# Kernel optimization log

Measured on AMD Instinct MI355X. Metric: run time of the kernel, lower is better.

## Reference

```python
import jax, jax.numpy as jnp
import numpy as np

C = 256
HEADS = 8
HEAD_DIM = C // HEADS
GROUPS = 8
EPS = 1e-5


def setup_inputs() -> dict:
    key = jax.random.key(0)
    ks = jax.random.split(key, 11)
    B, S = 2, 16
    s = 0.02
    return {
        "x": jax.random.normal(ks[0], (B, C, S, S, S), dtype=jnp.float32),
        "gn_w": jnp.ones((C,), jnp.float32),
        "gn_b": jnp.zeros((C,), jnp.float32),
        "wq": jax.random.normal(ks[1], (C, C), jnp.float32) * s,
        "bq": jnp.zeros((C,), jnp.float32),
        "wk": jax.random.normal(ks[2], (C, C), jnp.float32) * s,
        "bk": jnp.zeros((C,), jnp.float32),
        "wv": jax.random.normal(ks[3], (C, C), jnp.float32) * s,
        "bv": jnp.zeros((C,), jnp.float32),
        "wo": jax.random.normal(ks[4], (C, C), jnp.float32) * s,
        "bo": jnp.zeros((C,), jnp.float32),
    }


def _group_norm(x, w, b):
    # x: [B, C, D, H, W]; GroupNorm(8, C) with affine params
    B, Cc, D, H, W = x.shape
    xg = x.reshape(B, GROUPS, Cc // GROUPS, D, H, W)
    mu = jnp.mean(xg, axis=(2, 3, 4, 5), keepdims=True)
    var = jnp.mean(jnp.square(xg - mu), axis=(2, 3, 4, 5), keepdims=True)
    xn = ((xg - mu) * jax.lax.rsqrt(var + EPS)).reshape(B, Cc, D, H, W)
    return xn * w[None, :, None, None, None] + b[None, :, None, None, None]


def reference(x, gn_w, gn_b, wq, bq, wk, bk, wv, bv, wo, bo):
    B, Cc, D, H, W = x.shape
    N = D * H * W
    xn = _group_norm(x, gn_w, gn_b).reshape(B, Cc, N)  # [B,C,N]
    # 1x1x1 Conv3d == per-voxel linear: weight [out,in]
    Q = jnp.einsum("oc,bcn->bon", wq, xn) + bq[None, :, None]
    K = jnp.einsum("oc,bcn->bon", wk, xn) + bk[None, :, None]
    V = jnp.einsum("oc,bcn->bon", wv, xn) + bv[None, :, None]
    Q = Q.reshape(B, HEADS, HEAD_DIM, N)
    K = K.reshape(B, HEADS, HEAD_DIM, N)
    V = V.reshape(B, HEADS, HEAD_DIM, N)
    scale = np.sqrt(HEAD_DIM).astype(np.float32)
    attn = jnp.einsum("bhdn,bhdm->bhnm", Q, K) / scale
    attn = jax.nn.softmax(attn, axis=-1)
    out = jnp.einsum("bhnm,bhdm->bhdn", attn, V)  # [B,h,hd,N]
    out = out.reshape(B, Cc, N)
    out = jnp.einsum("oc,bcn->bon", wo, out) + bo[None, :, None]
    return x + out.reshape(B, Cc, D, H, W)
```

## Files before the change

### kernel.cpp

```cpp
#include <hip/hip_runtime.h>

#define B_   2
#define C_   256
#define N_   4096
#define H_   8
#define HD_  32
#define G_   8
#define CPG_ 32

typedef short short8 __attribute__((ext_vector_type(8)));
typedef short short4v __attribute__((ext_vector_type(4)));
typedef unsigned uint4v __attribute__((ext_vector_type(4)));
typedef float f32x4  __attribute__((ext_vector_type(4)));
typedef float f4     __attribute__((ext_vector_type(4)));

__device__ __forceinline__ float b2f(short s) {
    return __uint_as_float(((unsigned)(unsigned short)s) << 16);
}
__device__ __forceinline__ short f2b(float f) {
    unsigned u = __float_as_uint(f);
    unsigned r = (u + 0x7FFF + ((u >> 16) & 1)) >> 16;
    return (short)r;
}

__global__ __launch_bounds__(256) void gn_part(const float* __restrict__ x,
                                               float* __restrict__ part) {
    int blk = blockIdx.x;
    const f4* p = (const f4*)x + (size_t)(blk >> 6) * (CPG_ * N_ / 4) + (size_t)(blk & 63) * 512;
    float s = 0.f, ss = 0.f;
#pragma unroll
    for (int i = 0; i < 2; i++) {
        f4 v = p[threadIdx.x + i * 256];
#pragma unroll
        for (int j = 0; j < 4; j++) { float f = v[j]; s += f; ss += f * f; }
    }
#pragma unroll
    for (int off = 32; off > 0; off >>= 1) {
        s  += __shfl_down(s, off);
        ss += __shfl_down(ss, off);
    }
    __shared__ float rs[4], rss[4];
    int w = threadIdx.x >> 6;
    if ((threadIdx.x & 63) == 0) { rs[w] = s; rss[w] = ss; }
    __syncthreads();
    if (threadIdx.x == 0) {
        part[blk * 2]     = rs[0] + rs[1] + rs[2] + rs[3];
        part[blk * 2 + 1] = rss[0] + rss[1] + rss[2] + rss[3];
    }
}

__global__ __launch_bounds__(256) void wconv(const float* __restrict__ wq,
                                             const float* __restrict__ wk,
                                             const float* __restrict__ wv,
                                             const float* __restrict__ wo,
                                             short* __restrict__ wb) {
    int gid = blockIdx.x * 256 + threadIdx.x;
    int rid = gid >> 13;
    int off = (gid & 8191) * 8;
    const float* src = rid == 0 ? wq : (rid == 1 ? wk : (rid == 2 ? wv : wo));
    f4 a = *(const f4*)(src + off);
    f4 b = *(const f4*)(src + off + 4);
    short8 r;
#pragma unroll
    for (int j = 0; j < 4; j++) { r[j] = f2b(a[j]); r[j + 4] = f2b(b[j]); }
    *(short8*)&wb[(size_t)rid * 65536 + off] = r;
}

__global__ __launch_bounds__(256, 2) void gemm_qkv(
    const float* __restrict__ x,
    const float* __restrict__ gw, const float* __restrict__ gb,
    const float* __restrict__ part,
    const short* __restrict__ wb,
    const float* __restrict__ bq, const float* __restrict__ bk,
    const float* __restrict__ bv,
    short* __restrict__ q, short* __restrict__ kt, short* __restrict__ v) {
    int b = blockIdx.z;
    int o0 = blockIdx.y * 64, n0 = blockIdx.x * 64;
    const float mul = 0.17677669529663687f * 1.4426950408889634f;

    __shared__ short wl[3][64][40];
    __shared__ short xl[64][40];
    __shared__ float ga[256], gbb[256];
    __shared__ float mus[8], rstds[8];

    int tid = threadIdx.x;
    int w = tid >> 6, lane = tid & 63, li = lane & 15, quad = lane >> 4;
    int wr = w & 1, wc = w >> 1;

#pragma unroll
    for (int gi = 0; gi < 2; gi++) {
        int g = w * 2 + gi;
        const float* pp = &part[(size_t)(b * 8 + g) * 128 + lane * 2];
        float s = pp[0], ss = pp[1];
#pragma unroll
        for (int off = 32; off > 0; off >>= 1) {
            s  += __shfl_down(s, off);
            ss += __shfl_down(ss, off);
        }
        if (lane == 0) {
            const float inv = 1.f / (float)(CPG_ * N_);
            float mu = s * inv;
            float var = ss * inv - mu * mu;
            mus[g] = mu;
            rstds[g] = rsqrtf(var + 1e-5f);
        }
    }
    __syncthreads();
    {
        int c = tid, g = c >> 5;
        float a = rstds[g] * gw[c];
        ga[c]  = a;
        gbb[c] = gb[c] - mus[g] * a;
    }

    f32x4 aq[2][2], ak[2][2], av[2][2];
#pragma unroll
    for (int i = 0; i < 2; i++)
#pragma unroll
        for (int j = 0; j < 2; j++) {
            aq[i][j] = (f32x4){0.f, 0.f, 0.f, 0.f};
            ak[i][j] = (f32x4){0.f, 0.f, 0.f, 0.f};
            av[i][j] = (f32x4){0.f, 0.f, 0.f, 0.f};
        }

    int wrow = tid >> 2, wco = (tid & 3) << 3;
    int cpair = tid >> 4, l16 = tid & 15;
    __syncthreads();

    for (int k0 = 0; k0 < 256; k0 += 32) {
#pragma unroll
        for (int m = 0; m < 3; m++)
            *(short8*)&wl[m][wrow][wco] =
                *(const short8*)&wb[(size_t)m * 65536 + (size_t)(o0 + wrow) * 256 + k0 + wco];
        {
            int c0 = k0 + cpair * 2;
            float a0 = ga[c0],     b0c = gbb[c0];
            float a1 = ga[c0 + 1], b1c = gbb[c0 + 1];
            const float* xr0 = x + ((size_t)(b * 256 + c0)) * N_ + n0 + l16;
            const float* xr1 = xr0 + N_;
#pragma unroll
            for (int j = 0; j < 4; j++) {
                unsigned lo = (unsigned short)f2b(xr0[16 * j] * a0 + b0c);
                unsigned hi = (unsigned short)f2b(xr1[16 * j] * a1 + b1c);
                *(unsigned*)&xl[l16 + 16 * j][cpair * 2] = lo | (hi << 16);
            }
        }
        __syncthreads();

        short8 xf[2];
#pragma unroll
        for (int i = 0; i < 2; i++)
            xf[i] = *(short8*)&xl[wc * 32 + i * 16 + li][quad * 8];
#pragma unroll
        for (int j = 0; j < 2; j++) {
            short8 wfq = *(short8*)&wl[0][wr * 32 + j * 16 + li][quad * 8];
            short8 wfk = *(short8*)&wl[1][wr * 32 + j * 16 + li][quad * 8];
            short8 wfv = *(short8*)&wl[2][wr * 32 + j * 16 + li][quad * 8];
#pragma unroll
            for (int i = 0; i < 2; i++) {
                aq[i][j] = __builtin_amdgcn_mfma_f32_16x16x32_bf16(xf[i], wfq, aq[i][j], 0, 0, 0);
                ak[i][j] = __builtin_amdgcn_mfma_f32_16x16x32_bf16(xf[i], wfk, ak[i][j], 0, 0, 0);
                av[j][i] = __builtin_amdgcn_mfma_f32_16x16x32_bf16(wfv, xf[i], av[j][i], 0, 0, 0);
            }
        }
        __syncthreads();
    }

    {
        short* outp = q + (size_t)b * N_ * C_;
#pragma unroll
        for (int i = 0; i < 2; i++) {
            int nb_ = n0 + wc * 32 + i * 16 + quad * 4;
#pragma unroll
            for (int j = 0; j < 2; j++) {
                int o_ = o0 + wr * 32 + j * 16 + li;
                float bv_ = bq[o_];
#pragma unroll
                for (int r = 0; r < 4; r++)
                    outp[(size_t)(nb_ + r) * C_ + o_] = f2b((aq[i][j][r] + bv_) * mul);
            }
        }
    }
    {
#pragma unroll
        for (int i = 0; i < 2; i++) {
            int nb_ = n0 + wc * 32 + i * 16 + quad * 4;
#pragma unroll
            for (int j = 0; j < 2; j++) {
                int o_ = o0 + wr * 32 + j * 16 + li;
                int hh = o_ >> 5, d = o_ & 31;
                float bv_ = bk[o_];
                short* kdst = kt + ((size_t)(b * 8 + hh) * N_) * HD_ + d;
#pragma unroll
                for (int r = 0; r < 4; r++)
                    kdst[(size_t)(nb_ + r) * HD_] = f2b(ak[i][j][r] + bv_);
            }
        }
    }
    {
        short* outp = v + (size_t)b * C_ * N_;
#pragma unroll
        for (int j = 0; j < 2; j++) {
            int ob = o0 + wr * 32 + j * 16 + quad * 4;
#pragma unroll
            for (int i = 0; i < 2; i++) {
                int n_ = n0 + wc * 32 + i * 16 + li;
#pragma unroll
                for (int r = 0; r < 4; r++)
                    outp[(size_t)(ob + r) * N_ + n_] = f2b(av[j][i][r] + bv[ob + r]);
            }
        }
    }
}

__global__ __launch_bounds__(512) void flash(const short* __restrict__ q,
                                             const short* __restrict__ ktp,
                                             const short* __restrict__ v,
                                             short* __restrict__ aoT) {
    int bid = blockIdx.x;
    int xcd = bid & 7;
    int rest = bid >> 3;
    int bh = xcd * 2 + (rest & 1);
    int nb = rest >> 1;
    int b = bh >> 3, h = bh & 7;

    const short* QT = q   + (size_t)b * N_ * C_ + h * HD_;
    const short* KP = ktp + (size_t)bh * N_ * HD_;
    const short* V  = v   + ((size_t)b * C_ + h * HD_) * N_;
    short* O = aoT + (size_t)b * N_ * C_ + h * HD_;

    __shared__ short kl[2 * 2560];
    __shared__ short vl[2 * 2304];

    int tid = threadIdx.x, w = tid >> 6, lane = tid & 63, li = lane & 15, quad = lane >> 4;
    int n0w = nb * 256 + w * 32;

    short8 qf0 = *(const short8*)&QT[(size_t)(n0w + li) * 256 + quad * 8];
    short8 qf1 = *(const short8*)&QT[(size_t)(n0w + 16 + li) * 256 + quad * 8];

    f32x4 oa00 = (f32x4){0.f,0.f,0.f,0.f}, oa01 = oa00, oa10 = oa00, oa11 = oa00;
    float lr0 = 0.f, lr1 = 0.f;
    const f32x4 zero = (f32x4){0.f, 0.f, 0.f, 0.f};

    int krow = tid >> 3, kcol = (tid & 7) << 2;
    const short* kgp = KP + (size_t)krow * HD_ + kcol;
    int klo = krow * 40 + kcol;
    int vd = tid >> 4, g = tid & 15;
    int mbase = 32 * (g >> 3) + 16 * (g & 1) + 4 * ((g >> 1) & 3);
    const short* vgp = V + (size_t)vd * N_ + mbase;
    int vlo = vd * 72 + g * 4;

    short4v kst = *(const short4v*)kgp;
    short4v vst = *(const short4v*)vgp;

    f32x4 s0[4], s1[4];
    short8 vf[4];

    for (int t = 0; t < 64; ++t) {
        int buf = t & 1;
        *(short4v*)&kl[buf * 2560 + klo] = kst;
        *(short4v*)&vl[buf * 2304 + vlo] = vst;
        if (t < 63) {
            kst = *(const short4v*)(kgp + (size_t)(t + 1) * 64 * HD_);
            vst = *(const short4v*)(vgp + (t + 1) * 64);
        }
        __syncthreads();

        __builtin_amdgcn_s_setprio(1);
#pragma unroll
        for (int c = 0; c < 4; c++) {
            short8 kf = *(short8*)&kl[buf * 2560 + (c * 16 + li) * 40 + quad * 8];
            s0[c] = __builtin_amdgcn_mfma_f32_16x16x32_bf16(kf, qf0, zero, 0, 0, 0);
            s1[c] = __builtin_amdgcn_mfma_f32_16x16x32_bf16(kf, qf1, zero, 0, 0, 0);
        }
        __builtin_amdgcn_s_setprio(0);

        vf[0] = *(short8*)&vl[buf * 2304 + li * 72 + quad * 8];
        vf[1] = *(short8*)&vl[buf * 2304 + (16 + li) * 72 + quad * 8];
        vf[2] = *(short8*)&vl[buf * 2304 + li * 72 + 32 + quad * 8];
        vf[3] = *(short8*)&vl[buf * 2304 + (16 + li) * 72 + 32 + quad * 8];

        unsigned paw[8];
        float lp = 0.f;
#pragma unroll
        for (int c = 0; c < 4; c++) {
            float e0 = __builtin_amdgcn_exp2f(s0[c][0]);
            float e1 = __builtin_amdgcn_exp2f(s0[c][1]);
            float e2 = __builtin_amdgcn_exp2f(s0[c][2]);
            float e3 = __builtin_amdgcn_exp2f(s0[c][3]);
            lp += (e0 + e1) + (e2 + e3);
            paw[2 * c]     = __builtin_amdgcn_perm(__float_as_uint(e1), __float_as_uint(e0), 0x07060302);
            paw[2 * c + 1] = __builtin_amdgcn_perm(__float_as_uint(e3), __float_as_uint(e2), 0x07060302);
        }
        lr0 += lp;
        uint4v p0 = (uint4v){paw[0], paw[1], paw[2], paw[3]};
        uint4v p1 = (uint4v){paw[4], paw[5], paw[6], paw[7]};
        short8 a0 = __builtin_bit_cast(short8, p0);
        short8 a1 = __builtin_bit_cast(short8, p1);

        lp = 0.f;
#pragma unroll
        for (int c = 0; c < 4; c++) {
            float e0 = __builtin_amdgcn_exp2f(s1[c][0]);
            float e1 = __builtin_amdgcn_exp2f(s1[c][1]);
            float e2 = __builtin_amdgcn_exp2f(s1[c][2]);
            float e3 = __builtin_amdgcn_exp2f(s1[c][3]);
            lp += (e0 + e1) + (e2 + e3);
            paw[2 * c]     = __builtin_amdgcn_perm(__float_as_uint(e1), __float_as_uint(e0), 0x07060302);
            paw[2 * c + 1] = __builtin_amdgcn_perm(__float_as_uint(e3), __float_as_uint(e2), 0x07060302);
        }
        lr1 += lp;
        uint4v p2 = (uint4v){paw[0], paw[1], paw[2], paw[3]};
        uint4v p3 = (uint4v){paw[4], paw[5], paw[6], paw[7]};
        short8 a2 = __builtin_bit_cast(short8, p2);
        short8 a3 = __builtin_bit_cast(short8, p3);

        __builtin_amdgcn_s_setprio(1);
        oa00 = __builtin_amdgcn_mfma_f32_16x16x32_bf16(a0, vf[0], oa00, 0, 0, 0);
        oa01 = __builtin_amdgcn_mfma_f32_16x16x32_bf16(a0, vf[1], oa01, 0, 0, 0);
        oa00 = __builtin_amdgcn_mfma_f32_16x16x32_bf16(a1, vf[2], oa00, 0, 0, 0);
        oa01 = __builtin_amdgcn_mfma_f32_16x16x32_bf16(a1, vf[3], oa01, 0, 0, 0);
        oa10 = __builtin_amdgcn_mfma_f32_16x16x32_bf16(a2, vf[0], oa10, 0, 0, 0);
        oa11 = __builtin_amdgcn_mfma_f32_16x16x32_bf16(a2, vf[1], oa11, 0, 0, 0);
        oa10 = __builtin_amdgcn_mfma_f32_16x16x32_bf16(a3, vf[2], oa10, 0, 0, 0);
        oa11 = __builtin_amdgcn_mfma_f32_16x16x32_bf16(a3, vf[3], oa11, 0, 0, 0);
        __builtin_amdgcn_s_setprio(0);
    }

    lr0 += __shfl_xor(lr0, 16); lr0 += __shfl_xor(lr0, 32);
    lr1 += __shfl_xor(lr1, 16); lr1 += __shfl_xor(lr1, 32);
#pragma unroll
    for (int r = 0; r < 4; r++) {
        float ln0 = __shfl(lr0, quad * 4 + r);
        float inv0 = 1.f / ln0;
        size_t n_ = (size_t)(n0w + quad * 4 + r);
        O[n_ * 256 + li]      = f2b(oa00[r] * inv0);
        O[n_ * 256 + 16 + li] = f2b(oa01[r] * inv0);
        float ln1 = __shfl(lr1, quad * 4 + r);
        float inv1 = 1.f / ln1;
        size_t n2 = (size_t)(n0w + 16 + quad * 4 + r);
        O[n2 * 256 + li]      = f2b(oa10[r] * inv1);
        O[n2 * 256 + 16 + li] = f2b(oa11[r] * inv1);
    }
}

__global__ __launch_bounds__(256) void gemm_out(const short* __restrict__ wob,
                                                const float* __restrict__ bias,
                                                const short* __restrict__ aoT,
                                                const float* __restrict__ resid,
                                                float* __restrict__ out) {
    int b = blockIdx.z;
    const short* X = aoT + (size_t)b * N_ * C_;
    const float* R = resid + (size_t)b * C_ * N_;
    float* outp = out + (size_t)b * C_ * N_;

    __shared__ short wl[64][40];
    __shared__ short xl[64][40];

    int o0 = blockIdx.y * 64, n0 = blockIdx.x * 64;
    int tid = threadIdx.x;
    int w = tid >> 6, lane = tid & 63, li = lane & 15, quad = lane >> 4;
    int wr = w & 1, wc = w >> 1;

    f32x4 acc[2][2];
#pragma unroll
    for (int i = 0; i < 2; i++)
#pragma unroll
        for (int j = 0; j < 2; j++) acc[i][j] = (f32x4){0.f, 0.f, 0.f, 0.f};

    int row = tid >> 2, co = (tid & 3) << 3;
    for (int k0 = 0; k0 < 256; k0 += 32) {
        *(short8*)&wl[row][co] = *(const short8*)&wob[(size_t)(o0 + row) * 256 + k0 + co];
        *(short8*)&xl[row][co] = *(const short8*)&X[(size_t)(n0 + row) * 256 + k0 + co];
        __syncthreads();
        short8 af[2], bfr[2];
#pragma unroll
        for (int i = 0; i < 2; i++) af[i]  = *(short8*)&wl[wr * 32 + i * 16 + li][quad * 8];
#pragma unroll
        for (int j = 0; j < 2; j++) bfr[j] = *(short8*)&xl[wc * 32 + j * 16 + li][quad * 8];
#pragma unroll
        for (int i = 0; i < 2; i++)
#pragma unroll
            for (int j = 0; j < 2; j++)
                acc[i][j] = __builtin_amdgcn_mfma_f32_16x16x32_bf16(af[i], bfr[j], acc[i][j], 0, 0, 0);
        __syncthreads();
    }
#pragma unroll
    for (int i = 0; i < 2; i++) {
        int ob = o0 + wr * 32 + i * 16 + quad * 4;
#pragma unroll
        for (int j = 0; j < 2; j++) {
            int n_ = n0 + wc * 32 + j * 16 + li;
#pragma unroll
            for (int r = 0; r < 4; r++) {
                size_t idx = (size_t)(ob + r) * N_ + n_;
                outp[idx] = acc[i][j][r] + bias[ob + r] + R[idx];
            }
        }
    }
}

extern "C" void kernel_launch(void* const* d_in, const int* in_sizes, int n_in,
                              void* d_out, int out_size, void* d_ws, size_t ws_size,
                              hipStream_t stream) {
    const float* x  = (const float*)d_in[0];
    const float* gw = (const float*)d_in[1];
    const float* gb = (const float*)d_in[2];
    const float* wq = (const float*)d_in[3];
    const float* bq = (const float*)d_in[4];
    const float* wk = (const float*)d_in[5];
    const float* bk = (const float*)d_in[6];
    const float* wv = (const float*)d_in[7];
    const float* bv = (const float*)d_in[8];
    const float* wo = (const float*)d_in[9];
    const float* bo = (const float*)d_in[10];
    float* out = (float*)d_out;

    char* ws = (char*)d_ws;
    float* part = (float*)ws;
    const size_t TS = (size_t)B_ * N_ * C_;
    short* aoT = (short*)(ws + 16384);
    short* q   = aoT + TS;
    short* kt  = q + TS;
    short* v   = kt + TS;
    short* wb  = v + TS;

    gn_part<<<1024, 256, 0, stream>>>(x, part);
    wconv<<<128, 256, 0, stream>>>(wq, wk, wv, wo, wb);
    gemm_qkv<<<dim3(64, 4, 2), 256, 0, stream>>>(x, gw, gb, part, wb,
                                                 bq, bk, bv, q, kt, v);
    flash<<<256, 512, 0, stream>>>(q, kt, v, aoT);
    gemm_out<<<dim3(64, 4, 2), 256, 0, stream>>>(wb + 3 * 65536, bo, aoT, x, out);
}
```

Baseline: 147.7 us.

## Merge GN stats and weight conversion kernels; process two key tiles per flash iteration

Merges the group-norm partial-sum kernel and the weight bf16 conversion into one launch, branching on block index. In the flash attention kernel, each loop iteration now stages two 64-key tiles (128 keys) with double buffering, halving the number of barriers and iterations. The QK MFMAs for both tiles are issued back to back, and the second tile's exp/PV work can then overlap with them. It also adds a launch bound requesting 2 blocks per CU. The cost is doubled LDS use per block and higher register pressure from the extra score accumulators.

Result: no change. 147.2 us (-0.3%).

```diff
diff --git a/kernel.cpp b/kernel.cpp
--- a/kernel.cpp
+++ b/kernel.cpp
@@ -23,47 +23,48 @@
     return (short)r;
 }
 
-__global__ __launch_bounds__(256) void gn_part(const float* __restrict__ x,
-                                               float* __restrict__ part) {
+__global__ __launch_bounds__(256) void prep(const float* __restrict__ x,
+                                            float* __restrict__ part,
+                                            const float* __restrict__ wq,
+                                            const float* __restrict__ wk,
+                                            const float* __restrict__ wv,
+                                            const float* __restrict__ wo,
+                                            short* __restrict__ wb) {
     int blk = blockIdx.x;
-    const f4* p = (const f4*)x + (size_t)(blk >> 6) * (CPG_ * N_ / 4) + (size_t)(blk & 63) * 512;
-    float s = 0.f, ss = 0.f;
-#pragma unroll
-    for (int i = 0; i < 2; i++) {
-        f4 v = p[threadIdx.x + i * 256];
-#pragma unroll
-        for (int j = 0; j < 4; j++) { float f = v[j]; s += f; ss += f * f; }
-    }
-#pragma unroll
-    for (int off = 32; off > 0; off >>= 1) {
-        s  += __shfl_down(s, off);
-        ss += __shfl_down(ss, off);
-    }
-    __shared__ float rs[4], rss[4];
-    int w = threadIdx.x >> 6;
-    if ((threadIdx.x & 63) == 0) { rs[w] = s; rss[w] = ss; }
-    __syncthreads();
-    if (threadIdx.x == 0) {
-        part[blk * 2]     = rs[0] + rs[1] + rs[2] + rs[3];
-        part[blk * 2 + 1] = rss[0] + rss[1] + rss[2] + rss[3];
-    }
-}
-
-__global__ __launch_bounds__(256) void wconv(const float* __restrict__ wq,
-                                             const float* __restrict__ wk,
-                                             const float* __restrict__ wv,
-                                             const float* __restrict__ wo,
-                                             short* __restrict__ wb) {
-    int gid = blockIdx.x * 256 + threadIdx.x;
-    int rid = gid >> 13;
-    int off = (gid & 8191) * 8;
-    const float* src = rid == 0 ? wq : (rid == 1 ? wk : (rid == 2 ? wv : wo));
-    f4 a = *(const f4*)(src + off);
-    f4 b = *(const f4*)(src + off + 4);
-    short8 r;
-#pragma unroll
-    for (int j = 0; j < 4; j++) { r[j] = f2b(a[j]); r[j + 4] = f2b(b[j]); }
-    *(short8*)&wb[(size_t)rid * 65536 + off] = r;
+    if (blk < 1024) {
+        const f4* p = (const f4*)x + (size_t)(blk >> 6) * (CPG_ * N_ / 4) + (size_t)(blk & 63) * 512;
+        float s = 0.f, ss = 0.f;
+#pragma unroll
+        for (int i = 0; i < 2; i++) {
+            f4 v = p[threadIdx.x + i * 256];
+#pragma unroll
+            for (int j = 0; j < 4; j++) { float f = v[j]; s += f; ss += f * f; }
+        }
+#pragma unroll
+        for (int off = 32; off > 0; off >>= 1) {
+            s  += __shfl_down(s, off);
+            ss += __shfl_down(ss, off);
+        }
+        __shared__ float rs[4], rss[4];
+        int w = threadIdx.x >> 6;
+        if ((threadIdx.x & 63) == 0) { rs[w] = s; rss[w] = ss; }
+        __syncthreads();
+        if (threadIdx.x == 0) {
+            part[blk * 2]     = rs[0] + rs[1] + rs[2] + rs[3];
+            part[blk * 2 + 1] = rss[0] + rss[1] + rss[2] + rss[3];
+        }
+    } else {
+        int gid = (blk - 1024) * 256 + threadIdx.x;
+        int rid = gid >> 13;
+        int off = (gid & 8191) * 8;
+        const float* src = rid == 0 ? wq : (rid == 1 ? wk : (rid == 2 ? wv : wo));
+        f4 a = *(const f4*)(src + off);
+        f4 b = *(const f4*)(src + off + 4);
+        short8 r;
+#pragma unroll
+        for (int j = 0; j < 4; j++) { r[j] = f2b(a[j]); r[j + 4] = f2b(b[j]); }
+        *(short8*)&wb[(size_t)rid * 65536 + off] = r;
+    }
 }
 
 __global__ __launch_bounds__(256, 2) void gemm_qkv(
@@ -213,10 +214,31 @@
     }
 }
 
-__global__ __launch_bounds__(512) void flash(const short* __restrict__ q,
-                                             const short* __restrict__ ktp,
-                                             const short* __restrict__ v,
-                                             short* __restrict__ aoT) {
+#define EXPPACK(sx, lrx, A0, A1)                                          \
+    {                                                                     \
+        unsigned paw[8];                                                  \
+        float lp = 0.f;                                                   \
+        _Pragma("unroll")                                                 \
+        for (int c = 0; c < 4; c++) {                                     \
+            float e0 = __builtin_amdgcn_exp2f(sx[c][0]);                  \
+            float e1 = __builtin_amdgcn_exp2f(sx[c][1]);                  \
+            float e2 = __builtin_amdgcn_exp2f(sx[c][2]);                  \
+            float e3 = __builtin_amdgcn_exp2f(sx[c][3]);                  \
+            lp += (e0 + e1) + (e2 + e3);                                  \
+            paw[2 * c]     = __builtin_amdgcn_perm(__float_as_uint(e1), __float_as_uint(e0), 0x07060302); \
+            paw[2 * c + 1] = __builtin_amdgcn_perm(__float_as_uint(e3), __float_as_uint(e2), 0x07060302); \
+        }                                                                 \
+        lrx += lp;                                                        \
+        uint4v p0_ = (uint4v){paw[0], paw[1], paw[2], paw[3]};            \
+        uint4v p1_ = (uint4v){paw[4], paw[5], paw[6], paw[7]};            \
+        A0 = __builtin_bit_cast(short8, p0_);                             \
+        A1 = __builtin_bit_cast(short8, p1_);                             \
+    }
+
+__global__ __launch_bounds__(512, 2) void flash(const short* __restrict__ q,
+                                                const short* __restrict__ ktp,
+                                                const short* __restrict__ v,
+                                                short* __restrict__ aoT) {
     int bid = blockIdx.x;
     int xcd = bid & 7;
     int rest = bid >> 3;
@@ -229,8 +251,8 @@
     const short* V  = v   + ((size_t)b * C_ + h * HD_) * N_;
     short* O = aoT + (size_t)b * N_ * C_ + h * HD_;
 
-    __shared__ short kl[2 * 2560];
-    __shared__ short vl[2 * 2304];
+    __shared__ short kl[2 * 5120];
+    __shared__ short vl[2 * 4608];
 
     int tid = threadIdx.x, w = tid >> 6, lane = tid & 63, li = lane & 15, quad = lane >> 4;
     int n0w = nb * 256 + w * 32;
@@ -250,70 +272,72 @@
     const short* vgp = V + (size_t)vd * N_ + mbase;
     int vlo = vd * 72 + g * 4;
 
-    short4v kst = *(const short4v*)kgp;
-    short4v vst = *(const short4v*)vgp;
-
-    f32x4 s0[4], s1[4];
+    short4v kstA = *(const short4v*)kgp;
+    short4v kstB = *(const short4v*)(kgp + (size_t)64 * HD_);
+    short4v vstA = *(const short4v*)vgp;
+    short4v vstB = *(const short4v*)(vgp + 64);
+
+    f32x4 s0a[4], s1a[4], s0b[4], s1b[4];
     short8 vf[4];
 
-    for (int t = 0; t < 64; ++t) {
+    for (int t = 0; t < 32; ++t) {
         int buf = t & 1;
-        *(short4v*)&kl[buf * 2560 + klo] = kst;
-        *(short4v*)&vl[buf * 2304 + vlo] = vst;
-        if (t < 63) {
-            kst = *(const short4v*)(kgp + (size_t)(t + 1) * 64 * HD_);
-            vst = *(const short4v*)(vgp + (t + 1) * 64);
+        *(short4v*)&kl[buf * 5120 + klo] = kstA;
+        *(short4v*)&kl[buf * 5120 + 2560 + klo] = kstB;
+        *(short4v*)&vl[buf * 4608 + vlo] = vstA;
+        *(short4v*)&vl[buf * 4608 + 2304 + vlo] = vstB;
+        if (t < 31) {
+            const short* kq = kgp + (size_t)(t + 1) * 128 * HD_;
+            kstA = *(const short4v*)kq;
+            kstB = *(const short4v*)(kq + (size_t)64 * HD_);
+            const short* vq = vgp + (t + 1) * 128;
+            vstA = *(const short4v*)vq;
+            vstB = *(const short4v*)(vq + 64);
         }
         __syncthreads();
 
         __builtin_amdgcn_s_setprio(1);
 #pragma unroll
         for (int c = 0; c < 4; c++) {
-            short8 kf = *(short8*)&kl[buf * 2560 + (c * 16 + li) * 40 + quad * 8];
-            s0[c] = __builtin_amdgcn_mfma_f32_16x16x32_bf16(kf, qf0, zero, 0, 0, 0);
-            s1[c] = __builtin_amdgcn_mfma_f32_16x16x32_bf16(kf, qf1, zero, 0, 0, 0);
+            short8 kf = *(short8*)&kl[buf * 5120 + (c * 16 + li) * 40 + quad * 8];
+            s0a[c] = __builtin_amdgcn_mfma_f32_16x16x32_bf16(kf, qf0, zero, 0, 0, 0);
+            s1a[c] = __builtin_amdgcn_mfma_f32_16x16x32_bf16(kf, qf1, zero, 0, 0, 0);
+        }
+#pragma unroll
+        for (int c = 0; c < 4; c++) {
+            short8 kf = *(short8*)&kl[buf * 5120 + 2560 + (c * 16 + li) * 40 + quad * 8];
+            s0b[c] = __builtin_amdgcn_mfma_f32_16x16x32_bf16(kf, qf0, zero, 0, 0, 0);
+            s1b[c] = __builtin_amdgcn_mfma_f32_16x16x32_bf16(kf, qf1, zero, 0, 0, 0);
         }
         __builtin_amdgcn_s_setprio(0);
 
-        vf[0] = *(short8*)&vl[buf * 2304 + li * 72 + quad * 8];
-        vf[1] = *(short8*)&vl[buf * 2304 + (16 + li) * 72 + quad * 8];
-        vf[2] = *(short8*)&vl[buf * 2304 + li * 72 + 32 + quad * 8];
-        vf[3] = *(short8*)&vl[buf * 2304 + (16 + li) * 72 + 32 + quad * 8];
-
-        unsigned paw[8];
-        float lp = 0.f;
-#pragma unroll
-        for (int c = 0; c < 4; c++) {
-            float e0 = __builtin_amdgcn_exp2f(s0[c][0]);
-            float e1 = __builtin_amdgcn_exp2f(s0[c][1]);
-            float e2 = __builtin_amdgcn_exp2f(s0[c][2]);
-            float e3 = __builtin_amdgcn_exp2f(s0[c][3]);
-            lp += (e0 + e1) + (e2 + e3);
-            paw[2 * c]     = __builtin_amdgcn_perm(__float_as_uint(e1), __float_as_uint(e0), 0x07060302);
-            paw[2 * c + 1] = __builtin_amdgcn_perm(__float_as_uint(e3), __float_as_uint(e2), 0x07060302);
-        }
-        lr0 += lp;
-        uint4v p0 = (uint4v){paw[0], paw[1], paw[2], paw[3]};
-        uint4v p1 = (uint4v){paw[4], paw[5], paw[6], paw[7]};
-        short8 a0 = __builtin_bit_cast(short8, p0);
-        short8 a1 = __builtin_bit_cast(short8, p1);
-
-        lp = 0.f;
-#pragma unroll
-        for (int c = 0; c < 4; c++) {
-            float e0 = __builtin_amdgcn_exp2f(s1[c][0]);
-            float e1 = __builtin_amdgcn_exp2f(s1[c][1]);
-            float e2 = __builtin_amdgcn_exp2f(s1[c][2]);
-            float e3 = __builtin_amdgcn_exp2f(s1[c][3]);
-            lp += (e0 + e1) + (e2 + e3);
-            paw[2 * c]     = __builtin_amdgcn_perm(__float_as_uint(e1), __float_as_uint(e0), 0x07060302);
-            paw[2 * c + 1] = __builtin_amdgcn_perm(__float_as_uint(e3), __float_as_uint(e2), 0x07060302);
-        }
-        lr1 += lp;
-        uint4v p2 = (uint4v){paw[0], paw[1], paw[2], paw[3]};
-        uint4v p3 = (uint4v){paw[4], paw[5], paw[6], paw[7]};
-        short8 a2 = __builtin_bit_cast(short8, p2);
-        short8 a3 = __builtin_bit_cast(short8, p3);
+        vf[0] = *(short8*)&vl[buf * 4608 + li * 72 + quad * 8];
+        vf[1] = *(short8*)&vl[buf * 4608 + (16 + li) * 72 + quad * 8];
+        vf[2] = *(short8*)&vl[buf * 4608 + li * 72 + 32 + quad * 8];
+        vf[3] = *(short8*)&vl[buf * 4608 + (16 + li) * 72 + 32 + quad * 8];
+
+        short8 a0, a1, a2, a3;
+        EXPPACK(s0a, lr0, a0, a1);
+        EXPPACK(s1a, lr1, a2, a3);
+
+        __builtin_amdgcn_s_setprio(1);
+        oa00 = __builtin_amdgcn_mfma_f32_16x16x32_bf16(a0, vf[0], oa00, 0, 0, 0);
+        oa01 = __builtin_amdgcn_mfma_f32_16x16x32_bf16(a0, vf[1], oa01, 0, 0, 0);
+        oa00 = __builtin_amdgcn_mfma_f32_16x16x32_bf16(a1, vf[2], oa00, 0, 0, 0);
+        oa01 = __builtin_amdgcn_mfma_f32_16x16x32_bf16(a1, vf[3], oa01, 0, 0, 0);
+        oa10 = __builtin_amdgcn_mfma_f32_16x16x32_bf16(a2, vf[0], oa10, 0, 0, 0);
+        oa11 = __builtin_amdgcn_mfma_f32_16x16x32_bf16(a2, vf[1], oa11, 0, 0, 0);
+        oa10 = __builtin_amdgcn_mfma_f32_16x16x32_bf16(a3, vf[2], oa10, 0, 0, 0);
+        oa11 = __builtin_amdgcn_mfma_f32_16x16x32_bf16(a3, vf[3], oa11, 0, 0, 0);
+        __builtin_amdgcn_s_setprio(0);
+
+        vf[0] = *(short8*)&vl[buf * 4608 + 2304 + li * 72 + quad * 8];
+        vf[1] = *(short8*)&vl[buf * 4608 + 2304 + (16 + li) * 72 + quad * 8];
+        vf[2] = *(short8*)&vl[buf * 4608 + 2304 + li * 72 + 32 + quad * 8];
+        vf[3] = *(short8*)&vl[buf * 4608 + 2304 + (16 + li) * 72 + 32 + quad * 8];
+
+        EXPPACK(s0b, lr0, a0, a1);
+        EXPPACK(s1b, lr1, a2, a3);
 
         __builtin_amdgcn_s_setprio(1);
         oa00 = __builtin_amdgcn_mfma_f32_16x16x32_bf16(a0, vf[0], oa00, 0, 0, 0);
@@ -425,8 +449,7 @@
     short* v   = kt + TS;
     short* wb  = v + TS;
 
-    gn_part<<<1024, 256, 0, stream>>>(x, part);
-    wconv<<<128, 256, 0, stream>>>(wq, wk, wv, wo, wb);
+    prep<<<1152, 256, 0, stream>>>(x, part, wq, wk, wv, wo, wb);
     gemm_qkv<<<dim3(64, 4, 2), 256, 0, stream>>>(x, gw, gb, part, wb,
                                                  bq, bk, bv, q, kt, v);
     flash<<<256, 512, 0, stream>>>(q, kt, v, aoT);
```
